# Performance work log

Measured on AMD Instinct MI355X. Metric: run time of the kernel, lower is better.

Reference implementation:

```python
import jax, jax.numpy as jnp
import numpy as np

B, L, D = 4, 2048, 512
N_HEAD, D_K, D_V = 8, 64, 64
D_INNER, N_LAYERS, NUM_TYPES = 2048, 4, 22
PAD = 0
LN_EPS = 1e-6


def _layer_norm(x, g, b):
    m = jnp.mean(x, axis=-1, keepdims=True)
    v = jnp.mean((x - m) ** 2, axis=-1, keepdims=True)
    return (x - m) * jax.lax.rsqrt(v + LN_EPS) * g + b


def _temporal_enc(time, non_pad_mask):
    # position_vec[i] = 10000^(2*(i//2)/d_model)
    i = np.arange(D)
    pos_vec = jnp.asarray(10000.0 ** (2.0 * (i // 2) / D), dtype=jnp.float32)
    r = time[:, :, None] / pos_vec                      # [B,L,D]
    even = (jnp.arange(D) % 2) == 0
    r = jnp.where(even, jnp.sin(r), jnp.cos(r))
    return r * non_pad_mask


def setup_inputs() -> dict:
    key = jax.random.key(0)
    ks = jax.random.split(key, 20)
    event_type = jax.random.randint(ks[0], (B, L), 0, NUM_TYPES + 1)
    event_time = jnp.cumsum(jax.random.uniform(ks[1], (B, L), dtype=jnp.float32), axis=1)
    non_pad_mask = (event_type != PAD).astype(jnp.float32)[:, :, None]
    s = 0.02
    emb = jax.random.normal(ks[2], (NUM_TYPES + 1, D), dtype=jnp.float32) * s
    emb = emb.at[PAD].set(0.0)  # padding_idx row
    Wq = jax.random.normal(ks[3], (N_LAYERS, D, N_HEAD * D_K), dtype=jnp.float32) * s
    Wk = jax.random.normal(ks[4], (N_LAYERS, D, N_HEAD * D_K), dtype=jnp.float32) * s
    Wv = jax.random.normal(ks[5], (N_LAYERS, D, N_HEAD * D_V), dtype=jnp.float32) * s
    fc_w = jax.random.normal(ks[6], (N_LAYERS, N_HEAD * D_V, D), dtype=jnp.float32) * s
    fc_b = jnp.zeros((N_LAYERS, D), dtype=jnp.float32)
    ln1_g = jnp.ones((N_LAYERS, D), dtype=jnp.float32)
    ln1_b = jnp.zeros((N_LAYERS, D), dtype=jnp.float32)
    W1 = jax.random.normal(ks[7], (N_LAYERS, D, D_INNER), dtype=jnp.float32) * s
    b1 = jnp.zeros((N_LAYERS, D_INNER), dtype=jnp.float32)
    W2 = jax.random.normal(ks[8], (N_LAYERS, D_INNER, D), dtype=jnp.float32) * s
    b2 = jnp.zeros((N_LAYERS, D), dtype=jnp.float32)
    ln2_g = jnp.ones((N_LAYERS, D), dtype=jnp.float32)
    ln2_b = jnp.zeros((N_LAYERS, D), dtype=jnp.float32)
    return dict(event_type=event_type, event_time=event_time, non_pad_mask=non_pad_mask,
                emb=emb, Wq=Wq, Wk=Wk, Wv=Wv, fc_w=fc_w, fc_b=fc_b,
                ln1_g=ln1_g, ln1_b=ln1_b, W1=W1, b1=b1, W2=W2, b2=b2,
                ln2_g=ln2_g, ln2_b=ln2_b)


def reference(event_type, event_time, non_pad_mask, emb, Wq, Wk, Wv, fc_w, fc_b,
              ln1_g, ln1_b, W1, b1, W2, b2, ln2_g, ln2_b):
    # Attention mask. NOTE: in the source, slf_attn_mask_sparse is overwritten by
    # the keypad mask, so the effective mask is padding | causal.
    pad = (event_type == PAD)                                   # [B,L]
    keypad = pad[:, None, :]                                    # [B,1(L_q),L_k] broadcast
    subseq = jnp.triu(jnp.ones((L, L), dtype=bool), k=1)        # [L,L]
    mask = (keypad | subseq)[:, None, :, :]                     # [B,1,L,L] over heads

    tem = _temporal_enc(event_time, non_pad_mask)               # [B,L,D]
    x = emb[event_type]                                         # [B,L,D]
    scale = 1.0 / jnp.sqrt(jnp.float32(D_K))

    for l in range(N_LAYERS):
        x = x + tem
        # --- multi-head attention (post-LN, THP style) ---
        residual = x
        q = (x @ Wq[l]).reshape(B, L, N_HEAD, D_K)
        k = (x @ Wk[l]).reshape(B, L, N_HEAD, D_K)
        v = (x @ Wv[l]).reshape(B, L, N_HEAD, D_V)
        scores = jnp.einsum('bqhd,bkhd->bhqk', q, k) * scale    # [B,H,L,L]
        scores = jnp.where(mask, -1e9, scores)
        attn = jax.nn.softmax(scores, axis=-1)
        out = jnp.einsum('bhqk,bkhd->bqhd', attn, v).reshape(B, L, N_HEAD * D_V)
        out = out @ fc_w[l] + fc_b[l] + residual
        x = _layer_norm(out, ln1_g[l], ln1_b[l])
        x = x * non_pad_mask
        # --- position-wise FFN (exact GELU, post-LN) ---
        residual = x
        h = jax.nn.gelu(x @ W1[l] + b1[l], approximate=False)
        y = h @ W2[l] + b2[l] + residual
        x = _layer_norm(y, ln2_g[l], ln2_b[l])
        x = x * non_pad_mask
    return x
```

## Files before the change

### kernel.cpp

```cpp
#include <hip/hip_runtime.h>
#include <math.h>

#define BB 4
#define LL 2048
#define DD 512
#define NH 8
#define DINNER 2048
#define NLAYERS 4
#define MM (BB * LL)

typedef __attribute__((ext_vector_type(8))) __bf16 bf16x8;
typedef __attribute__((ext_vector_type(4))) float f32x4;

__device__ __forceinline__ unsigned short f2b(float f) {
  union { __bf16 h; unsigned short u; } v;
  v.h = (__bf16)f;
  return v.u;
}
__device__ __forceinline__ float b2f(unsigned short h) {
  union { unsigned u; float f; } v; v.u = ((unsigned)h) << 16; return v.f;
}
__device__ __forceinline__ unsigned pk2(float lo, float hi) {
  return (unsigned)f2b(lo) | ((unsigned)f2b(hi) << 16);
}
__device__ __forceinline__ float exp2f_fast(float x) {
  float r; asm("v_exp_f32 %0, %1" : "=v"(r) : "v"(x)); return r;
}

__device__ __forceinline__ void gload16(const void* g, void* l) {
  __builtin_amdgcn_global_load_lds(
      (const __attribute__((address_space(1))) void*)g,
      (__attribute__((address_space(3))) void*)l, 16, 0, 0);
}

__global__ __launch_bounds__(512) void init_kernel(
    const int* __restrict__ etype, const float* __restrict__ etime,
    const float* __restrict__ npm, const float* __restrict__ emb,
    float* __restrict__ tem, float* __restrict__ xa,
    unsigned short* __restrict__ xab) {
  int row = blockIdx.x;
  int d = threadIdx.x;
  float t = etime[row];
  float mask = npm[row];
  int dd = d & ~1;
  float pv = expf(9.210340371976184f * ((float)dd * (1.0f / (float)DD)));
  float r = t / pv;
  float val = (d & 1) ? cosf(r) : sinf(r);
  float tv = val * mask;
  tem[(size_t)row * DD + d] = tv;
  int ty = etype[row];
  float a = emb[(size_t)ty * DD + d] + tv;
  xa[(size_t)row * DD + d] = a;
  xab[(size_t)row * DD + d] = f2b(a);
}

__global__ __launch_bounds__(256) void wtrans_kernel(
    const float* __restrict__ in, unsigned short* __restrict__ out,
    int K, int N, long in_ls, long out_ls) {
  __shared__ float t[32][33];
  int l = blockIdx.z;
  int n0 = blockIdx.x * 32, k0 = blockIdx.y * 32;
  int tx = threadIdx.x & 31, ty = threadIdx.x >> 5;
  const float* ip = in + (size_t)l * in_ls;
  unsigned short* op = out + (size_t)l * out_ls;
#pragma unroll
  for (int r = ty; r < 32; r += 8)
    t[r][tx] = ip[(size_t)(k0 + r) * N + n0 + tx];
  __syncthreads();
#pragma unroll
  for (int r = ty; r < 32; r += 8)
    op[(size_t)(n0 + r) * K + k0 + tx] = f2b(t[tx][r]);
}

template <int BM, bool BIAS, bool RES, bool GELU_, bool OBF16>
__global__ __launch_bounds__(256) void gemm_kernel(
    const unsigned short* __restrict__ A, const unsigned short* __restrict__ WT,
    const float* __restrict__ bias, const float* __restrict__ res, int ldres,
    void* __restrict__ Cv, int ldc, int M, int N, int K) {
  __shared__ unsigned short As[2][BM * 32];
  __shared__ unsigned short Bs[2][128 * 32];
  constexpr int NT = (BM == 128) ? 4 : 2;
  int tid = threadIdx.x;
  int w = tid >> 6, l = tid & 63;
  int li = l & 15, g = l >> 4;
  int nwg = gridDim.x;
  int bid = blockIdx.x;
  int wg = (bid & 7) * (nwg >> 3) + (bid >> 3);
  int gx = N >> 7;
  int row0 = (wg / gx) * BM, col0 = (wg % gx) * 128;
  int wm = (BM == 128) ? (w & 1) * 64 : 0;
  int wnb = (BM == 128) ? (w >> 1) * 64 : w * 32;
  f32x4 acc[4][NT];
#pragma unroll
  for (int i = 0; i < 4; i++)
#pragma unroll
    for (int j = 0; j < NT; j++) acc[i][j] = (f32x4){0.f, 0.f, 0.f, 0.f};

  int lr = l >> 2;
  int lc = (l & 3) ^ (lr & 3);

  auto stage = [&](int bb, int kb) {
    int k0 = kb * 32;
    if (BM == 128) {
#pragma unroll
      for (int i = 0; i < 2; i++) {
        int ai = w * 2 + i;
        gload16(A + (size_t)(row0 + ai * 16 + lr) * K + k0 + lc * 8,
                &As[bb][ai * 512]);
        gload16(WT + (size_t)(col0 + ai * 16 + lr) * K + k0 + lc * 8,
                &Bs[bb][ai * 512]);
      }
    } else {
      gload16(A + (size_t)(row0 + w * 16 + lr) * K + k0 + lc * 8,
              &As[bb][w * 512]);
#pragma unroll
      for (int i = 0; i < 2; i++) {
        int bi = w * 2 + i;
        gload16(WT + (size_t)(col0 + bi * 16 + lr) * K + k0 + lc * 8,
                &Bs[bb][bi * 512]);
      }
    }
  };

  int nk = K >> 5;
  stage(0, 0);
  __syncthreads();
  int buf = 0;
  for (int kb = 0; kb < nk; kb++) {
    if (kb + 1 < nk) stage(buf ^ 1, kb + 1);
    bf16x8 af[4], bf_[NT];
#pragma unroll
    for (int mt = 0; mt < 4; mt++) {
      int r = wm + mt * 16 + li;
      af[mt] = *(const bf16x8*)&As[buf][r * 32 + ((g ^ (r & 3)) * 8)];
    }
#pragma unroll
    for (int nt = 0; nt < NT; nt++) {
      int r = wnb + nt * 16 + li;
      bf_[nt] = *(const bf16x8*)&Bs[buf][r * 32 + ((g ^ (r & 3)) * 8)];
    }
#pragma unroll
    for (int mt = 0; mt < 4; mt++)
#pragma unroll
      for (int nt = 0; nt < NT; nt++)
        acc[mt][nt] = __builtin_amdgcn_mfma_f32_16x16x32_bf16(
            af[mt], bf_[nt], acc[mt][nt], 0, 0, 0);
    __syncthreads();
    buf ^= 1;
  }
#pragma unroll
  for (int mt = 0; mt < 4; mt++) {
#pragma unroll
    for (int nt = 0; nt < NT; nt++) {
#pragma unroll
      for (int r = 0; r < 4; r++) {
        int row = row0 + wm + mt * 16 + g * 4 + r;
        int col = col0 + wnb + nt * 16 + li;
        float v = acc[mt][nt][r];
        if (BIAS) v += bias[col];
        if (RES) v += res[(size_t)row * ldres + col];
        if (GELU_) v = 0.5f * v * (1.0f + erff(v * 0.70710678118654752f));
        if (OBF16)
          ((unsigned short*)Cv)[(size_t)row * ldc + col] = f2b(v);
        else
          ((float*)Cv)[(size_t)row * ldc + col] = v;
      }
    }
  }
}

__global__ __launch_bounds__(256) void vtrans_kernel(
    const unsigned short* __restrict__ qkv, unsigned short* __restrict__ vT) {
  __shared__ unsigned short t[64][65];
  int bh = blockIdx.y;
  int b = bh >> 3, h = bh & 7;
  int l0 = blockIdx.x * 64;
  int tid = threadIdx.x;
  int c = tid & 63, p = tid >> 6;
#pragma unroll
  for (int r = p; r < 64; r += 4)
    t[r][c] = qkv[(size_t)(b * LL + l0 + r) * 1536 + 1024 + h * 64 + c];
  __syncthreads();
#pragma unroll
  for (int r = p; r < 64; r += 4)
    vT[((size_t)bh * 64 + r) * LL + l0 + c] = t[c][r];
}

__global__ __launch_bounds__(256) void meanv_kernel(
    const unsigned short* __restrict__ vT, float* __restrict__ meanV) {
  __shared__ float red[256];
  int bh = blockIdx.x;
  int tid = threadIdx.x;
  int d = tid >> 2, p = tid & 3;
  const unsigned short* vp = vT + ((size_t)bh * 64 + d) * LL;
  float s = 0.f;
  for (int i = p * 512; i < p * 512 + 512; i++) s += b2f(vp[i]);
  red[tid] = s;
  __syncthreads();
  if (p == 0)
    meanV[bh * 64 + d] =
        (red[tid] + red[tid + 1] + red[tid + 2] + red[tid + 3]) *
        (1.0f / (float)LL);
}

__global__ __launch_bounds__(256) void attn_kernel(
    const unsigned short* __restrict__ qkv, const unsigned short* __restrict__ vT,
    const int* __restrict__ etype, unsigned short* __restrict__ opart,
    float* __restrict__ ml) {
  __shared__ unsigned short Ks[2][64 * 64];
  __shared__ unsigned short Ps[64][72];
  int hwbid = blockIdx.x;
  int work = (hwbid & 7) * 256 + (hwbid >> 3);
  int bh = work >> 6;
  int rem = work & 63;
  int qt = 31 - (rem >> 1);
  int half = rem & 1;
  int h = bh & 7, b = bh >> 3;
  int q0 = qt * 64;
  int nt = qt + 1;
  int ha = (nt + 1) >> 1;
  int j0 = half ? ha : 0;
  int j1 = half ? nt : ha;
  int pidx = (bh * 32 + qt) * 2 + half;
  int tid = threadIdx.x, w = tid >> 6, l = tid & 63;
  int g = l >> 4, li = l & 15;
  const float SC = 0.125f * 1.44269504f;

  f32x4 o[4];
#pragma unroll
  for (int n = 0; n < 4; n++) o[n] = (f32x4){0.f, 0.f, 0.f, 0.f};
  float mreg[4], lreg[4];
#pragma unroll
  for (int r = 0; r < 4; r++) { mreg[r] = -3.0e38f; lreg[r] = 0.f; }

  if (j0 < j1) {
    const unsigned short* qrp =
        qkv + (size_t)(b * LL + q0 + w * 16 + li) * 1536 + h * 64;
    bf16x8 aq0 = *(const bf16x8*)&qrp[g * 8];
    bf16x8 aq1 = *(const bf16x8*)&qrp[32 + g * 8];

#pragma unroll
    for (int e = 0; e < 2; e++) {
      int idx = e * 256 + tid;
      int r = idx >> 3;
      int src = (l & 7) ^ (r & 7);
      gload16(
          qkv + (size_t)(b * LL + j0 * 64 + r) * 1536 + 512 + h * 64 + src * 8,
          &Ks[0][(e * 256 + w * 64) * 8]);
    }
    __syncthreads();

    int cur = 0;
    for (int j = j0; j < j1; j++) {
      int k0 = j << 6;
      if (j + 1 < j1) {
#pragma unroll
        for (int e = 0; e < 2; e++) {
          int idx = e * 256 + tid;
          int r = idx >> 3;
          int src = (l & 7) ^ (r & 7);
          gload16(qkv + (size_t)(b * LL + k0 + 64 + r) * 1536 + 512 + h * 64 +
                      src * 8,
                  &Ks[cur ^ 1][(e * 256 + w * 64) * 8]);
        }
      }
      bf16x8 bv0[4], bv1[4];
      float pb[4];
#pragma unroll
      for (int n = 0; n < 4; n++) {
        const unsigned short* vp =
            vT + ((size_t)(bh * 64 + n * 16 + li)) * LL + k0;
        bv0[n] = *(const bf16x8*)&vp[g * 8];
        bv1[n] = *(const bf16x8*)&vp[32 + g * 8];
        pb[n] = (etype[b * LL + k0 + n * 16 + li] == 0) ? -1.0e9f : 0.f;
      }
      f32x4 s[4];
#pragma unroll
      for (int n = 0; n < 4; n++) {
        int rK = n * 16 + li;
        const unsigned short* kb = &Ks[cur][rK * 64];
        bf16x8 bk0 = *(const bf16x8*)&kb[(g ^ (rK & 7)) * 8];
        bf16x8 bk1 = *(const bf16x8*)&kb[((g + 4) ^ (rK & 7)) * 8];
        f32x4 a = (f32x4){0.f, 0.f, 0.f, 0.f};
        __builtin_amdgcn_s_setprio(1);
        a = __builtin_amdgcn_mfma_f32_16x16x32_bf16(aq0, bk0, a, 0, 0, 0);
        a = __builtin_amdgcn_mfma_f32_16x16x32_bf16(aq1, bk1, a, 0, 0, 0);
        __builtin_amdgcn_s_setprio(0);
        s[n] = a;
      }
      if (j == qt) {
#pragma unroll
        for (int n = 0; n < 4; n++) {
          int key = k0 + n * 16 + li;
#pragma unroll
          for (int r = 0; r < 4; r++) {
            int qrow = q0 + w * 16 + g * 4 + r;
            float sv = fmaf(s[n][r], SC, pb[n]);
            if (key > qrow) sv = -1.0e9f;
            s[n][r] = sv;
          }
        }
      } else {
#pragma unroll
        for (int n = 0; n < 4; n++)
#pragma unroll
          for (int r = 0; r < 4; r++) s[n][r] = fmaf(s[n][r], SC, pb[n]);
      }
      float pm[4], corr[4], psum[4];
#pragma unroll
      for (int r = 0; r < 4; r++)
        pm[r] = fmaxf(fmaxf(s[0][r], s[1][r]), fmaxf(s[2][r], s[3][r]));
#pragma unroll
      for (int msk = 1; msk <= 8; msk <<= 1)
#pragma unroll
        for (int r = 0; r < 4; r++)
          pm[r] = fmaxf(pm[r], __shfl_xor(pm[r], msk, 64));
#pragma unroll
      for (int r = 0; r < 4; r++) {
        float mnew = fmaxf(mreg[r], pm[r]);
        corr[r] = exp2f_fast(mreg[r] - mnew);
        mreg[r] = mnew;
        float ps = 0.f;
#pragma unroll
        for (int n = 0; n < 4; n++) {
          float p = exp2f_fast(s[n][r] - mnew);
          s[n][r] = p;
          ps += p;
        }
        psum[r] = ps;
      }
#pragma unroll
      for (int msk = 1; msk <= 8; msk <<= 1)
#pragma unroll
        for (int r = 0; r < 4; r++) psum[r] += __shfl_xor(psum[r], msk, 64);
#pragma unroll
      for (int r = 0; r < 4; r++) lreg[r] = lreg[r] * corr[r] + psum[r];
#pragma unroll
      for (int n = 0; n < 4; n++)
#pragma unroll
        for (int r = 0; r < 4; r++)
          Ps[w * 16 + g * 4 + r][n * 16 + li] = f2b(s[n][r]);
#pragma unroll
      for (int n = 0; n < 4; n++)
#pragma unroll
        for (int r = 0; r < 4; r++) o[n][r] *= corr[r];
      bf16x8 ap0 = *(const bf16x8*)&Ps[w * 16 + li][g * 8];
      bf16x8 ap1 = *(const bf16x8*)&Ps[w * 16 + li][32 + g * 8];
      __builtin_amdgcn_s_setprio(1);
#pragma unroll
      for (int n = 0; n < 4; n++) {
        o[n] = __builtin_amdgcn_mfma_f32_16x16x32_bf16(ap0, bv0[n], o[n], 0, 0, 0);
        o[n] = __builtin_amdgcn_mfma_f32_16x16x32_bf16(ap1, bv1[n], o[n], 0, 0, 0);
      }
      __builtin_amdgcn_s_setprio(0);
      __syncthreads();
      cur ^= 1;
    }
  }
#pragma unroll
  for (int r = 0; r < 4; r++) {
    int qrl = w * 16 + g * 4 + r;
    float inv = (lreg[r] > 0.f) ? 1.0f / lreg[r] : 0.f;
#pragma unroll
    for (int n = 0; n < 4; n++)
      opart[((size_t)pidx * 64 + qrl) * 64 + n * 16 + li] = f2b(o[n][r] * inv);
    if (li == 0) {
      ml[(size_t)pidx * 128 + qrl] = mreg[r];
      ml[(size_t)pidx * 128 + 64 + qrl] = lreg[r];
    }
  }
}

__global__ __launch_bounds__(256) void amerge_kernel(
    const unsigned short* __restrict__ opart, const float* __restrict__ ml,
    const float* __restrict__ meanV, unsigned short* __restrict__ ao) {
  int blk = blockIdx.x;
  int bh = blk >> 5, qt = blk & 31;
  int b = bh >> 3, h = bh & 7;
  int tid = threadIdx.x;
  int d = tid & 63;
  int pA = blk * 2, pB = blk * 2 + 1;
  for (int rr = tid >> 6; rr < 64; rr += 4) {
    float mA = ml[(size_t)pA * 128 + rr], lA = ml[(size_t)pA * 128 + 64 + rr];
    float mB = ml[(size_t)pB * 128 + rr], lB = ml[(size_t)pB * 128 + 64 + rr];
    float m = fmaxf(mA, mB);
    float v;
    if (m <= -1.0e8f) {
      v = meanV[bh * 64 + d];
    } else {
      float acc = 0.f, wsum = 0.f;
      if (lA > 0.f) {
        float wA = exp2f_fast(mA - m) * lA;
        acc += b2f(opart[((size_t)pA * 64 + rr) * 64 + d]) * wA;
        wsum += wA;
      }
      if (lB > 0.f) {
        float wB = exp2f_fast(mB - m) * lB;
        acc += b2f(opart[((size_t)pB * 64 + rr) * 64 + d]) * wB;
        wsum += wB;
      }
      v = acc / wsum;
    }
    int qr = qt * 64 + rr;
    ao[(size_t)(b * LL + qr) * DD + h * 64 + d] = f2b(v);
  }
}

template <bool ADDTEM>
__global__ __launch_bounds__(256) void ln_kernel(
    const unsigned short* __restrict__ in, const float* __restrict__ g,
    const float* __restrict__ bta, const float* __restrict__ npm,
    const float* __restrict__ tem, float* __restrict__ out,
    float* __restrict__ out2, unsigned short* __restrict__ out_bf) {
  __shared__ float red[4];
  int row = blockIdx.x;
  int tid = threadIdx.x;
  unsigned u = ((const unsigned*)(in + (size_t)row * DD))[tid];
  float v0 = b2f((unsigned short)u), v1 = b2f((unsigned short)(u >> 16));
  int e0 = tid * 2, e1 = tid * 2 + 1;
  float s = v0 + v1;
#pragma unroll
  for (int o = 32; o > 0; o >>= 1) s += __shfl_down(s, o, 64);
  if ((tid & 63) == 0) red[tid >> 6] = s;
  __syncthreads();
  float mean = (red[0] + red[1] + red[2] + red[3]) * (1.0f / (float)DD);
  float d0 = v0 - mean, d1 = v1 - mean;
  float sq = d0 * d0 + d1 * d1;
#pragma unroll
  for (int o = 32; o > 0; o >>= 1) sq += __shfl_down(sq, o, 64);
  __syncthreads();
  if ((tid & 63) == 0) red[tid >> 6] = sq;
  __syncthreads();
  float var = (red[0] + red[1] + red[2] + red[3]) * (1.0f / (float)DD);
  float rstd = rsqrtf(var + 1e-6f);
  float m = npm[row];
  float o0 = (d0 * rstd * g[e0] + bta[e0]) * m;
  float o1 = (d1 * rstd * g[e1] + bta[e1]) * m;
  ((float2*)(out + (size_t)row * DD))[tid] = make_float2(o0, o1);
  if (ADDTEM) {
    float2 tv = ((const float2*)(tem + (size_t)row * DD))[tid];
    float a0 = o0 + tv.x, a1 = o1 + tv.y;
    ((float2*)(out2 + (size_t)row * DD))[tid] = make_float2(a0, a1);
    ((unsigned*)(out_bf + (size_t)row * DD))[tid] = pk2(a0, a1);
  } else {
    ((unsigned*)(out_bf + (size_t)row * DD))[tid] = pk2(o0, o1);
  }
}

extern "C" void kernel_launch(void* const* d_in, const int* in_sizes, int n_in,
                              void* d_out, int out_size, void* d_ws,
                              size_t ws_size, hipStream_t stream) {
  const int* etype = (const int*)d_in[0];
  const float* etime = (const float*)d_in[1];
  const float* npm = (const float*)d_in[2];
  const float* emb = (const float*)d_in[3];
  const float* Wq = (const float*)d_in[4];
  const float* Wk = (const float*)d_in[5];
  const float* Wv = (const float*)d_in[6];
  const float* fc_w = (const float*)d_in[7];
  const float* fc_b = (const float*)d_in[8];
  const float* ln1_g = (const float*)d_in[9];
  const float* ln1_b = (const float*)d_in[10];
  const float* W1 = (const float*)d_in[11];
  const float* b1 = (const float*)d_in[12];
  const float* W2 = (const float*)d_in[13];
  const float* b2 = (const float*)d_in[14];
  const float* ln2_g = (const float*)d_in[15];
  const float* ln2_b = (const float*)d_in[16];

  float* x = (float*)d_out;
  char* ws = (char*)d_ws;
  const size_t SZF = (size_t)MM * DD * sizeof(float);
  const size_t SZB = (size_t)MM * DD * sizeof(short);
  float* tem = (float*)ws; ws += SZF;
  float* xa  = (float*)ws; ws += SZF;
  unsigned short* xab = (unsigned short*)ws; ws += SZB;
  unsigned short* xbf = (unsigned short*)ws; ws += SZB;
  unsigned short* qkv = (unsigned short*)ws; ws += (size_t)MM * 1536 * 2;
  unsigned short* vT  = (unsigned short*)ws; ws += (size_t)BB * NH * 64 * LL * 2;
  unsigned short* ao  = (unsigned short*)ws; ws += SZB;
  unsigned short* hb  = (unsigned short*)ws; ws += (size_t)MM * DINNER * 2;
  unsigned short* ybb = (unsigned short*)ws; ws += SZB;
  unsigned short* qkvT = (unsigned short*)ws; ws += (size_t)NLAYERS * 1536 * 512 * 2;
  unsigned short* fcT  = (unsigned short*)ws; ws += (size_t)NLAYERS * 512 * 512 * 2;
  unsigned short* W1T  = (unsigned short*)ws; ws += (size_t)NLAYERS * 2048 * 512 * 2;
  unsigned short* W2T  = (unsigned short*)ws; ws += (size_t)NLAYERS * 512 * 2048 * 2;
  float* meanV = (float*)ws; ws += BB * NH * 64 * sizeof(float);
  unsigned short* opart = (unsigned short*)ws; ws += (size_t)2048 * 64 * 64 * 2;
  float* ml = (float*)ws; ws += (size_t)2048 * 128 * sizeof(float);

  init_kernel<<<MM, 512, 0, stream>>>(etype, etime, npm, emb, tem, xa, xab);

  wtrans_kernel<<<dim3(16, 16, NLAYERS), 256, 0, stream>>>(
      Wq, qkvT + 0 * 512 * 512, 512, 512, 512L * 512, 1536L * 512);
  wtrans_kernel<<<dim3(16, 16, NLAYERS), 256, 0, stream>>>(
      Wk, qkvT + 1 * 512 * 512, 512, 512, 512L * 512, 1536L * 512);
  wtrans_kernel<<<dim3(16, 16, NLAYERS), 256, 0, stream>>>(
      Wv, qkvT + 2 * 512 * 512, 512, 512, 512L * 512, 1536L * 512);
  wtrans_kernel<<<dim3(16, 16, NLAYERS), 256, 0, stream>>>(
      fc_w, fcT, 512, 512, 512L * 512, 512L * 512);
  wtrans_kernel<<<dim3(64, 16, NLAYERS), 256, 0, stream>>>(
      W1, W1T, 512, 2048, 512L * 2048, 2048L * 512);
  wtrans_kernel<<<dim3(16, 64, NLAYERS), 256, 0, stream>>>(
      W2, W2T, 2048, 512, 2048L * 512, 512L * 2048);

  for (int l = 0; l < NLAYERS; l++) {
    gemm_kernel<128, false, false, false, true><<<64 * 12, 256, 0, stream>>>(
        xab, qkvT + (size_t)l * 1536 * 512, nullptr, nullptr, 0, qkv, 1536,
        MM, 1536, 512);

    vtrans_kernel<<<dim3(32, 32), 256, 0, stream>>>(qkv, vT);
    meanv_kernel<<<BB * NH, 256, 0, stream>>>(vT, meanV);
    attn_kernel<<<2048, 256, 0, stream>>>(qkv, vT, etype, opart, ml);
    amerge_kernel<<<1024, 256, 0, stream>>>(opart, ml, meanV, ao);

    gemm_kernel<64, true, true, false, true><<<128 * 4, 256, 0, stream>>>(
        ao, fcT + (size_t)l * 512 * 512, fc_b + (size_t)l * 512, xa, 512, ybb,
        512, MM, 512, 512);
    ln_kernel<false><<<MM, 256, 0, stream>>>(
        ybb, ln1_g + (size_t)l * 512, ln1_b + (size_t)l * 512, npm, nullptr, x,
        nullptr, xbf);

    gemm_kernel<128, true, false, true, true><<<64 * 16, 256, 0, stream>>>(
        xbf, W1T + (size_t)l * 2048 * 512, b1 + (size_t)l * 2048, nullptr, 0,
        hb, 2048, MM, 2048, 512);
    gemm_kernel<64, true, true, false, true><<<128 * 4, 256, 0, stream>>>(
        hb, W2T + (size_t)l * 512 * 2048, b2 + (size_t)l * 512, x, 512, ybb,
        512, MM, 512, 2048);
    ln_kernel<true><<<MM, 256, 0, stream>>>(
        ybb, ln2_g + (size_t)l * 512, ln2_b + (size_t)l * 512, npm, tem, x, xa,
        xab);
  }
}
```

Before: 1.043 ms.

## Split-K the W2 FFN GEMM and fuse partial reduction into layernorm

The second FFN GEMM (K=2048) is split into four K-slices, launching four times as many workgroups. Each slice writes bf16 partials. A new layernorm kernel sums the partials, adds bias and residual, then normalizes and adds the temporal encoding. This targets low occupancy and long serial K loops in that GEMM. The cost is extra memory traffic for the partial buffers and some precision loss from rounding partials to bf16.

```diff
diff --git a/kernel.cpp b/kernel.cpp
--- a/kernel.cpp
+++ b/kernel.cpp
@@ -72,7 +72,7 @@
     op[(size_t)(n0 + r) * K + k0 + tx] = f2b(t[tx][r]);
 }
 
-template <int BM, bool BIAS, bool RES, bool GELU_, bool OBF16>
+template <int BM, bool BIAS, bool RES, bool GELU_, bool OBF16, int NS = 1>
 __global__ __launch_bounds__(256) void gemm_kernel(
     const unsigned short* __restrict__ A, const unsigned short* __restrict__ WT,
     const float* __restrict__ bias, const float* __restrict__ res, int ldres,
@@ -87,7 +87,15 @@
   int bid = blockIdx.x;
   int wg = (bid & 7) * (nwg >> 3) + (bid >> 3);
   int gx = N >> 7;
+  int split = 0;
+  if (NS > 1) {
+    int items = (M / BM) * gx;
+    split = wg / items;
+    wg -= split * items;
+  }
   int row0 = (wg / gx) * BM, col0 = (wg % gx) * 128;
+  int kbeg = (NS > 1) ? split * (K / NS) : 0;
+  size_t splitoff = (size_t)split * M * ldc;
   int wm = (BM == 128) ? (w & 1) * 64 : 0;
   int wnb = (BM == 128) ? (w >> 1) * 64 : w * 32;
   f32x4 acc[4][NT];
@@ -100,7 +108,7 @@
   int lc = (l & 3) ^ (lr & 3);
 
   auto stage = [&](int bb, int kb) {
-    int k0 = kb * 32;
+    int k0 = kbeg + kb * 32;
     if (BM == 128) {
 #pragma unroll
       for (int i = 0; i < 2; i++) {
@@ -122,7 +130,7 @@
     }
   };
 
-  int nk = K >> 5;
+  int nk = (K / NS) >> 5;
   stage(0, 0);
   __syncthreads();
   int buf = 0;
@@ -161,9 +169,9 @@
         if (RES) v += res[(size_t)row * ldres + col];
         if (GELU_) v = 0.5f * v * (1.0f + erff(v * 0.70710678118654752f));
         if (OBF16)
-          ((unsigned short*)Cv)[(size_t)row * ldc + col] = f2b(v);
+          ((unsigned short*)Cv)[splitoff + (size_t)row * ldc + col] = f2b(v);
         else
-          ((float*)Cv)[(size_t)row * ldc + col] = v;
+          ((float*)Cv)[splitoff + (size_t)row * ldc + col] = v;
       }
     }
   }
@@ -406,12 +414,10 @@
   }
 }
 
-template <bool ADDTEM>
 __global__ __launch_bounds__(256) void ln_kernel(
     const unsigned short* __restrict__ in, const float* __restrict__ g,
     const float* __restrict__ bta, const float* __restrict__ npm,
-    const float* __restrict__ tem, float* __restrict__ out,
-    float* __restrict__ out2, unsigned short* __restrict__ out_bf) {
+    float* __restrict__ out, unsigned short* __restrict__ out_bf) {
   __shared__ float red[4];
   int row = blockIdx.x;
   int tid = threadIdx.x;
@@ -437,14 +443,55 @@
   float o0 = (d0 * rstd * g[e0] + bta[e0]) * m;
   float o1 = (d1 * rstd * g[e1] + bta[e1]) * m;
   ((float2*)(out + (size_t)row * DD))[tid] = make_float2(o0, o1);
-  if (ADDTEM) {
-    float2 tv = ((const float2*)(tem + (size_t)row * DD))[tid];
-    float a0 = o0 + tv.x, a1 = o1 + tv.y;
-    ((float2*)(out2 + (size_t)row * DD))[tid] = make_float2(a0, a1);
-    ((unsigned*)(out_bf + (size_t)row * DD))[tid] = pk2(a0, a1);
-  } else {
-    ((unsigned*)(out_bf + (size_t)row * DD))[tid] = pk2(o0, o1);
-  }
+  ((unsigned*)(out_bf + (size_t)row * DD))[tid] = pk2(o0, o1);
+}
+
+__global__ __launch_bounds__(256) void ln2f_kernel(
+    const unsigned short* __restrict__ part,
+    const float* __restrict__ bias, const float* __restrict__ resx,
+    const float* __restrict__ g, const float* __restrict__ bta,
+    const float* __restrict__ npm, const float* __restrict__ tem,
+    float* __restrict__ out, float* __restrict__ out2,
+    unsigned short* __restrict__ out_bf) {
+  __shared__ float red[4];
+  int row = blockIdx.x;
+  int tid = threadIdx.x;
+  int e0 = tid * 2, e1 = tid * 2 + 1;
+  const size_t ro = (size_t)row * DD;
+  unsigned u0 = ((const unsigned*)(part + 0 * (size_t)MM * DD + ro))[tid];
+  unsigned u1 = ((const unsigned*)(part + 1 * (size_t)MM * DD + ro))[tid];
+  unsigned u2 = ((const unsigned*)(part + 2 * (size_t)MM * DD + ro))[tid];
+  unsigned u3 = ((const unsigned*)(part + 3 * (size_t)MM * DD + ro))[tid];
+  float2 rv = ((const float2*)(resx + ro))[tid];
+  float v0 = b2f((unsigned short)u0) + b2f((unsigned short)u1) +
+             b2f((unsigned short)u2) + b2f((unsigned short)u3) + bias[e0] +
+             rv.x;
+  float v1 = b2f((unsigned short)(u0 >> 16)) + b2f((unsigned short)(u1 >> 16)) +
+             b2f((unsigned short)(u2 >> 16)) + b2f((unsigned short)(u3 >> 16)) +
+             bias[e1] + rv.y;
+  float s = v0 + v1;
+#pragma unroll
+  for (int o = 32; o > 0; o >>= 1) s += __shfl_down(s, o, 64);
+  if ((tid & 63) == 0) red[tid >> 6] = s;
+  __syncthreads();
+  float mean = (red[0] + red[1] + red[2] + red[3]) * (1.0f / (float)DD);
+  float d0 = v0 - mean, d1 = v1 - mean;
+  float sq = d0 * d0 + d1 * d1;
+#pragma unroll
+  for (int o = 32; o > 0; o >>= 1) sq += __shfl_down(sq, o, 64);
+  __syncthreads();
+  if ((tid & 63) == 0) red[tid >> 6] = sq;
+  __syncthreads();
+  float var = (red[0] + red[1] + red[2] + red[3]) * (1.0f / (float)DD);
+  float rstd = rsqrtf(var + 1e-6f);
+  float m = npm[row];
+  float o0 = (d0 * rstd * g[e0] + bta[e0]) * m;
+  float o1 = (d1 * rstd * g[e1] + bta[e1]) * m;
+  ((float2*)(out + ro))[tid] = make_float2(o0, o1);
+  float2 tv = ((const float2*)(tem + ro))[tid];
+  float a0 = o0 + tv.x, a1 = o1 + tv.y;
+  ((float2*)(out2 + ro))[tid] = make_float2(a0, a1);
+  ((unsigned*)(out_bf + ro))[tid] = pk2(a0, a1);
 }
 
 extern "C" void kernel_launch(void* const* d_in, const int* in_sizes, int n_in,
@@ -481,6 +528,7 @@
   unsigned short* ao  = (unsigned short*)ws; ws += SZB;
   unsigned short* hb  = (unsigned short*)ws; ws += (size_t)MM * DINNER * 2;
   unsigned short* ybb = (unsigned short*)ws; ws += SZB;
+  unsigned short* pbuf = (unsigned short*)ws; ws += 4 * SZB;
   unsigned short* qkvT = (unsigned short*)ws; ws += (size_t)NLAYERS * 1536 * 512 * 2;
   unsigned short* fcT  = (unsigned short*)ws; ws += (size_t)NLAYERS * 512 * 512 * 2;
   unsigned short* W1T  = (unsigned short*)ws; ws += (size_t)NLAYERS * 2048 * 512 * 2;
@@ -517,18 +565,17 @@
     gemm_kernel<64, true, true, false, true><<<128 * 4, 256, 0, stream>>>(
         ao, fcT + (size_t)l * 512 * 512, fc_b + (size_t)l * 512, xa, 512, ybb,
         512, MM, 512, 512);
-    ln_kernel<false><<<MM, 256, 0, stream>>>(
-        ybb, ln1_g + (size_t)l * 512, ln1_b + (size_t)l * 512, npm, nullptr, x,
-        nullptr, xbf);
+    ln_kernel<<<MM, 256, 0, stream>>>(ybb, ln1_g + (size_t)l * 512,
+                                      ln1_b + (size_t)l * 512, npm, x, xbf);
 
     gemm_kernel<128, true, false, true, true><<<64 * 16, 256, 0, stream>>>(
         xbf, W1T + (size_t)l * 2048 * 512, b1 + (size_t)l * 2048, nullptr, 0,
         hb, 2048, MM, 2048, 512);
-    gemm_kernel<64, true, true, false, true><<<128 * 4, 256, 0, stream>>>(
-        hb, W2T + (size_t)l * 512 * 2048, b2 + (size_t)l * 512, x, 512, ybb,
-        512, MM, 512, 2048);
-    ln_kernel<true><<<MM, 256, 0, stream>>>(
-        ybb, ln2_g + (size_t)l * 512, ln2_b + (size_t)l * 512, npm, tem, x, xa,
-        xab);
-  }
-}
+    gemm_kernel<64, false, false, false, true, 4><<<2048, 256, 0, stream>>>(
+        hb, W2T + (size_t)l * 512 * 2048, nullptr, nullptr, 0, pbuf, 512, MM,
+        512, 2048);
+    ln2f_kernel<<<MM, 256, 0, stream>>>(
+        pbuf, b2 + (size_t)l * 512, x, ln2_g + (size_t)l * 512,
+        ln2_b + (size_t)l * 512, npm, tem, x, xa, xab);
+  }
+}
```

After: 1.063 ms. Within noise of the previous version (+1.9%).
